# Kernel optimization log

Measured on AMD Instinct MI355X. Metric: run time of the kernel, lower is better.

The kernel has to match this reference:

```python
import jax, jax.numpy as jnp
import numpy as np

B, E, K = 512, 4096, 1024      # batch, emb_dim, key_dim
M, L = 1024, 32                # mem_size, prompt_length
TOP_K = 4
EPS = 1e-12


def _l2norm(x, axis=-1):
    n = jnp.linalg.norm(x, axis=axis, keepdims=True)
    return x / jnp.maximum(n, EPS)


def setup_inputs() -> dict:
    key = jax.random.key(0)
    k1, k2, k3, k4 = jax.random.split(key, 4)
    return {
        "x_query": jax.random.normal(k1, (B, E), dtype=jnp.float32),
        "W_proj": jax.random.normal(k2, (K, E), dtype=jnp.float32) * 0.02,
        "prompt_memory": jax.random.normal(k3, (M, L, E), dtype=jnp.float32) * 0.02,
        "prompt_keys": jax.random.normal(k4, (M, K), dtype=jnp.float32) * 0.02,
        "top_k": TOP_K,
    }


def reference(x_query, W_proj, prompt_memory, prompt_keys, top_k):
    # x_proj = Linear(emb_dim -> key_dim, no bias): x @ W.T
    x_proj = jnp.einsum("be,ke->bk", x_query, W_proj)          # [B, K]
    x_norm = _l2norm(x_proj)                                     # [B, K]
    key_norm = _l2norm(prompt_keys)                              # [M, K]
    sim = jnp.einsum("bk,mk->bm", x_norm, key_norm)             # [B, M]
    _, idx = jax.lax.top_k(sim, top_k)                           # [B, top_k]
    sel_prompts = prompt_memory[idx]                             # [B, top_k, L, E]
    sel_keys = _l2norm(prompt_keys[idx], axis=2)                 # [B, top_k, K]
    refined = jnp.einsum("bk,btk->bt", x_norm, sel_keys)        # [B, top_k]
    w = jax.nn.softmax(refined, axis=1)                          # [B, top_k]
    # softmax-weighted sum over selected prompts
    out = jnp.einsum("btle,bt->ble", sel_prompts, w)            # [B, L, E]
    return out
```

## Files before the change

### kernel.cpp

```cpp
#include <hip/hip_runtime.h>
#include <math.h>

#define BDIM 512
#define EDIM 4096
#define KDIM 1024
#define MDIM 1024
#define LDIM 32
#define TOPK 4
#define EPSF 1e-12f

typedef __attribute__((ext_vector_type(8))) short short8;
typedef __attribute__((ext_vector_type(4))) float f32x4;

struct us4 { ushort x, y, z, w; };

__device__ inline ushort f2bf_rn(float x) {
    union { float f; unsigned u; } v; v.f = x;
    unsigned r = (v.u + 0x7FFF + ((v.u >> 16) & 1)) >> 16;
    return (ushort)r;
}
__device__ inline float bf2f(ushort h) {
    union { unsigned u; float f; } v; v.u = ((unsigned)h) << 16;
    return v.f;
}

__global__ __launch_bounds__(256)
void split_all_kernel(const float* __restrict__ xq, const float* __restrict__ wp,
                      const float* __restrict__ pk,
                      ushort* __restrict__ xq_h, ushort* __restrict__ xq_l,
                      ushort* __restrict__ wp_h, ushort* __restrict__ wp_l,
                      ushort* __restrict__ pk_h, ushort* __restrict__ pk_l,
                      float* __restrict__ kn)
{
    const int blk = blockIdx.x;
    const int t = threadIdx.x;
    const float* src; ushort* hi; ushort* lo; int base;
    bool do_norm = false; int rowbase = 0;
    if (blk < 512)       { src = xq; hi = xq_h; lo = xq_l; base = blk * 1024; }
    else if (blk < 1536) { src = wp; hi = wp_h; lo = wp_l; base = (blk - 512) * 1024; }
    else                 { src = pk; hi = pk_h; lo = pk_l; base = (blk - 1536) * 1024;
                           do_norm = true; rowbase = (blk - 1536) * 4; }

    __shared__ float wsum[4];
    const int lane = t & 63, wwid = t >> 6;

    #pragma unroll
    for (int it = 0; it < 4; ++it) {
        const int i = base + it * 256 + t;
        float4 v = ((const float4*)src)[i];
        us4 h, l;
        h.x = f2bf_rn(v.x); l.x = f2bf_rn(v.x - bf2f(h.x));
        h.y = f2bf_rn(v.y); l.y = f2bf_rn(v.y - bf2f(h.y));
        h.z = f2bf_rn(v.z); l.z = f2bf_rn(v.z - bf2f(h.z));
        h.w = f2bf_rn(v.w); l.w = f2bf_rn(v.w - bf2f(h.w));
        ((us4*)hi)[i] = h;
        ((us4*)lo)[i] = l;

        if (do_norm) {
            float sq = v.x * v.x + v.y * v.y + v.z * v.z + v.w * v.w;
            #pragma unroll
            for (int off = 32; off > 0; off >>= 1) sq += __shfl_down(sq, off, 64);
            __syncthreads();
            if (lane == 0) wsum[wwid] = sq;
            __syncthreads();
            if (t == 0)
                kn[rowbase + it] = sqrtf(wsum[0] + wsum[1] + wsum[2] + wsum[3]);
        }
    }
}

__global__ __launch_bounds__(256)
void gemm1_kernel(const ushort* __restrict__ Ah, const ushort* __restrict__ Al,
                  const ushort* __restrict__ Bh, const ushort* __restrict__ Bl,
                  float* __restrict__ Cp)
{
    __shared__ ushort ldsA[2][2][64][40];
    __shared__ ushort ldsB[2][2][128][40];

    const int t  = threadIdx.x;
    const int bn = blockIdx.x, bm = blockIdx.y, kz = blockIdx.z;
    const int srow = t >> 2, sg = t & 3;
    const int Kc = EDIM / 4;

    const size_t aoff  = (size_t)(bm * 64 + srow) * EDIM + kz * Kc + sg * 8;
    const size_t boff0 = (size_t)(bn * 128 + srow) * EDIM + kz * Kc + sg * 8;
    const size_t boff1 = (size_t)(bn * 128 + 64 + srow) * EDIM + kz * Kc + sg * 8;

    const int lane = t & 63, wid = t >> 6;
    const int wr = wid >> 1, wc = wid & 1;
    const int fr = lane & 15, fg = lane >> 4;

    f32x4 acc[2][4];
    #pragma unroll
    for (int i = 0; i < 2; ++i)
        #pragma unroll
        for (int j = 0; j < 4; ++j)
            acc[i][j] = (f32x4){0.f, 0.f, 0.f, 0.f};

    short8 pAh = *(const short8*)(Ah + aoff);
    short8 pAl = *(const short8*)(Al + aoff);
    short8 pBh0 = *(const short8*)(Bh + boff0);
    short8 pBl0 = *(const short8*)(Bl + boff0);
    short8 pBh1 = *(const short8*)(Bh + boff1);
    short8 pBl1 = *(const short8*)(Bl + boff1);

    *(short8*)(&ldsA[0][0][srow][sg * 8]) = pAh;
    *(short8*)(&ldsA[0][1][srow][sg * 8]) = pAl;
    *(short8*)(&ldsB[0][0][srow][sg * 8]) = pBh0;
    *(short8*)(&ldsB[0][1][srow][sg * 8]) = pBl0;
    *(short8*)(&ldsB[0][0][64 + srow][sg * 8]) = pBh1;
    *(short8*)(&ldsB[0][1][64 + srow][sg * 8]) = pBl1;

    int p = 0;
    for (int k0 = 0; k0 < Kc; k0 += 32) {
        const bool more = (k0 + 32 < Kc);
        if (more) {
            pAh = *(const short8*)(Ah + aoff + k0 + 32);
            pAl = *(const short8*)(Al + aoff + k0 + 32);
            pBh0 = *(const short8*)(Bh + boff0 + k0 + 32);
            pBl0 = *(const short8*)(Bl + boff0 + k0 + 32);
            pBh1 = *(const short8*)(Bh + boff1 + k0 + 32);
            pBl1 = *(const short8*)(Bl + boff1 + k0 + 32);
        }
        __syncthreads();

        short8 ah[2], al[2], bh[4], bl[4];
        #pragma unroll
        for (int i = 0; i < 2; ++i) {
            ah[i] = *(const short8*)(&ldsA[p][0][wr * 32 + i * 16 + fr][fg * 8]);
            al[i] = *(const short8*)(&ldsA[p][1][wr * 32 + i * 16 + fr][fg * 8]);
        }
        #pragma unroll
        for (int j = 0; j < 4; ++j) {
            bh[j] = *(const short8*)(&ldsB[p][0][wc * 64 + j * 16 + fr][fg * 8]);
            bl[j] = *(const short8*)(&ldsB[p][1][wc * 64 + j * 16 + fr][fg * 8]);
        }
        #pragma unroll
        for (int i = 0; i < 2; ++i)
            #pragma unroll
            for (int j = 0; j < 4; ++j) {
                acc[i][j] = __builtin_amdgcn_mfma_f32_16x16x32_bf16(ah[i], bh[j], acc[i][j], 0, 0, 0);
                acc[i][j] = __builtin_amdgcn_mfma_f32_16x16x32_bf16(ah[i], bl[j], acc[i][j], 0, 0, 0);
                acc[i][j] = __builtin_amdgcn_mfma_f32_16x16x32_bf16(al[i], bh[j], acc[i][j], 0, 0, 0);
            }

        if (more) {
            *(short8*)(&ldsA[p ^ 1][0][srow][sg * 8]) = pAh;
            *(short8*)(&ldsA[p ^ 1][1][srow][sg * 8]) = pAl;
            *(short8*)(&ldsB[p ^ 1][0][srow][sg * 8]) = pBh0;
            *(short8*)(&ldsB[p ^ 1][1][srow][sg * 8]) = pBl0;
            *(short8*)(&ldsB[p ^ 1][0][64 + srow][sg * 8]) = pBh1;
            *(short8*)(&ldsB[p ^ 1][1][64 + srow][sg * 8]) = pBl1;
        }
        p ^= 1;
    }

    float* Cz = Cp + (size_t)kz * BDIM * KDIM;
    #pragma unroll
    for (int i = 0; i < 2; ++i)
        #pragma unroll
        for (int j = 0; j < 4; ++j)
            #pragma unroll
            for (int q = 0; q < 4; ++q) {
                int orow = bm * 64 + wr * 32 + i * 16 + (lane >> 4) * 4 + q;
                int ocol = bn * 128 + wc * 64 + j * 16 + (lane & 15);
                Cz[(size_t)orow * KDIM + ocol] = acc[i][j][q];
            }
}

__global__ __launch_bounds__(256)
void gemm2_kernel(const ushort* __restrict__ Ah, const ushort* __restrict__ Al,
                  const ushort* __restrict__ Bh, const ushort* __restrict__ Bl,
                  float* __restrict__ Cp)
{
    __shared__ ushort lds[2][4][64][40];

    const int t  = threadIdx.x;
    const int bn = blockIdx.x, bm = blockIdx.y, kz = blockIdx.z;
    const int srow = t >> 2, sg = t & 3;
    const int Kc = KDIM / 2;

    const size_t aoff = (size_t)(bm * 64 + srow) * KDIM + kz * Kc + sg * 8;
    const size_t boff = (size_t)(bn * 64 + srow) * KDIM + kz * Kc + sg * 8;

    const int lane = t & 63, wid = t >> 6;
    const int wr = wid >> 1, wc = wid & 1;
    const int fr = lane & 15, fg = lane >> 4;

    f32x4 acc[2][2];
    #pragma unroll
    for (int i = 0; i < 2; ++i)
        #pragma unroll
        for (int j = 0; j < 2; ++j)
            acc[i][j] = (f32x4){0.f, 0.f, 0.f, 0.f};

    short8 pA0 = *(const short8*)(Ah + aoff);
    short8 pA1 = *(const short8*)(Al + aoff);
    short8 pB0 = *(const short8*)(Bh + boff);
    short8 pB1 = *(const short8*)(Bl + boff);

    *(short8*)(&lds[0][0][srow][sg * 8]) = pA0;
    *(short8*)(&lds[0][1][srow][sg * 8]) = pA1;
    *(short8*)(&lds[0][2][srow][sg * 8]) = pB0;
    *(short8*)(&lds[0][3][srow][sg * 8]) = pB1;

    int p = 0;
    for (int k0 = 0; k0 < Kc; k0 += 32) {
        const bool more = (k0 + 32 < Kc);
        if (more) {
            pA0 = *(const short8*)(Ah + aoff + k0 + 32);
            pA1 = *(const short8*)(Al + aoff + k0 + 32);
            pB0 = *(const short8*)(Bh + boff + k0 + 32);
            pB1 = *(const short8*)(Bl + boff + k0 + 32);
        }
        __syncthreads();

        short8 ah[2], al[2], bh[2], bl[2];
        #pragma unroll
        for (int i = 0; i < 2; ++i) {
            ah[i] = *(const short8*)(&lds[p][0][wr * 32 + i * 16 + fr][fg * 8]);
            al[i] = *(const short8*)(&lds[p][1][wr * 32 + i * 16 + fr][fg * 8]);
            bh[i] = *(const short8*)(&lds[p][2][wc * 32 + i * 16 + fr][fg * 8]);
            bl[i] = *(const short8*)(&lds[p][3][wc * 32 + i * 16 + fr][fg * 8]);
        }
        #pragma unroll
        for (int i = 0; i < 2; ++i)
            #pragma unroll
            for (int j = 0; j < 2; ++j) {
                acc[i][j] = __builtin_amdgcn_mfma_f32_16x16x32_bf16(ah[i], bh[j], acc[i][j], 0, 0, 0);
                acc[i][j] = __builtin_amdgcn_mfma_f32_16x16x32_bf16(ah[i], bl[j], acc[i][j], 0, 0, 0);
                acc[i][j] = __builtin_amdgcn_mfma_f32_16x16x32_bf16(al[i], bh[j], acc[i][j], 0, 0, 0);
            }

        if (more) {
            *(short8*)(&lds[p ^ 1][0][srow][sg * 8]) = pA0;
            *(short8*)(&lds[p ^ 1][1][srow][sg * 8]) = pA1;
            *(short8*)(&lds[p ^ 1][2][srow][sg * 8]) = pB0;
            *(short8*)(&lds[p ^ 1][3][srow][sg * 8]) = pB1;
        }
        p ^= 1;
    }

    float* Cz = Cp + (size_t)kz * BDIM * MDIM;
    #pragma unroll
    for (int i = 0; i < 2; ++i)
        #pragma unroll
        for (int j = 0; j < 2; ++j)
            #pragma unroll
            for (int q = 0; q < 4; ++q) {
                int orow = bm * 64 + wr * 32 + i * 16 + (lane >> 4) * 4 + q;
                int ocol = bn * 64 + wc * 32 + j * 16 + (lane & 15);
                Cz[(size_t)orow * MDIM + ocol] = acc[i][j][q];
            }
}

__global__ __launch_bounds__(256)
void reduce_split_norm_kernel(const float* __restrict__ Cp,
                              ushort* __restrict__ xh, ushort* __restrict__ xl,
                              float* __restrict__ xn)
{
    const int b = blockIdx.x;
    const int i = b * 256 + threadIdx.x;
    const int n4 = BDIM * KDIM / 4;

    float4 s = ((const float4*)Cp)[i];
    #pragma unroll
    for (int z = 1; z < 4; ++z) {
        float4 v = ((const float4*)Cp)[(size_t)z * n4 + i];
        s.x += v.x; s.y += v.y; s.z += v.z; s.w += v.w;
    }

    us4 h, l;
    h.x = f2bf_rn(s.x); l.x = f2bf_rn(s.x - bf2f(h.x));
    h.y = f2bf_rn(s.y); l.y = f2bf_rn(s.y - bf2f(h.y));
    h.z = f2bf_rn(s.z); l.z = f2bf_rn(s.z - bf2f(h.z));
    h.w = f2bf_rn(s.w); l.w = f2bf_rn(s.w - bf2f(h.w));
    ((us4*)xh)[i] = h;
    ((us4*)xl)[i] = l;

    float sq = s.x * s.x + s.y * s.y + s.z * s.z + s.w * s.w;
    #pragma unroll
    for (int off = 32; off > 0; off >>= 1) sq += __shfl_down(sq, off, 64);
    __shared__ float wsum[4];
    const int lane = threadIdx.x & 63, wwid = threadIdx.x >> 6;
    if (lane == 0) wsum[wwid] = sq;
    __syncthreads();
    if (threadIdx.x == 0)
        xn[b] = sqrtf(wsum[0] + wsum[1] + wsum[2] + wsum[3]);
}

__device__ inline bool tk_better(float x, int ix, float y, int iy) {
    return (x > y) || (x == y && ix < iy);
}
__device__ inline void tk_insert(float (&v)[4], int (&id)[4], float x, int m) {
    if (tk_better(x, m, v[3], id[3])) {
        v[3] = x; id[3] = m;
        if (tk_better(v[3], id[3], v[2], id[2])) {
            float tv = v[2]; int ti = id[2]; v[2] = v[3]; id[2] = id[3]; v[3] = tv; id[3] = ti;
            if (tk_better(v[2], id[2], v[1], id[1])) {
                tv = v[1]; ti = id[1]; v[1] = v[2]; id[1] = id[2]; v[2] = tv; id[2] = ti;
                if (tk_better(v[1], id[1], v[0], id[0])) {
                    tv = v[0]; ti = id[0]; v[0] = v[1]; id[0] = id[1]; v[1] = tv; id[1] = ti;
                }
            }
        }
    }
}
__global__ __launch_bounds__(256)
void topk_scale_kernel(const float* __restrict__ Cp2, const float* __restrict__ xn,
                       const float* __restrict__ kn,
                       int* __restrict__ topi, float* __restrict__ topw)
{
    const int b = blockIdx.x, t = threadIdx.x;
    const int lane = t & 63, wid = t >> 6;
    const float sb = 1.f / fmaxf(xn[b], EPSF);
    const float* r0 = Cp2 + (size_t)b * MDIM;
    const float* r1 = Cp2 + (size_t)BDIM * MDIM + (size_t)b * MDIM;

    float v[4] = {-INFINITY, -INFINITY, -INFINITY, -INFINITY};
    int id[4] = {-1, -1, -1, -1};
    #pragma unroll
    for (int j = 0; j < MDIM / 256; ++j) {
        int m = wid * 256 + j * 64 + lane;
        float s = (r0[m] + r1[m]) * sb / fmaxf(kn[m], EPSF);
        tk_insert(v, id, s, m);
    }
    for (int off = 32; off >= 1; off >>= 1) {
        float pv[4]; int pi[4];
        #pragma unroll
        for (int q = 0; q < 4; ++q) {
            pv[q] = __shfl_xor(v[q], off, 64);
            pi[q] = __shfl_xor(id[q], off, 64);
        }
        #pragma unroll
        for (int q = 0; q < 4; ++q) tk_insert(v, id, pv[q], pi[q]);
    }

    __shared__ float sv[4][4];
    __shared__ int   si[4][4];
    if (lane == 0) {
        #pragma unroll
        for (int q = 0; q < 4; ++q) { sv[wid][q] = v[q]; si[wid][q] = id[q]; }
    }
    __syncthreads();
    if (t == 0) {
        float fv[4] = {-INFINITY, -INFINITY, -INFINITY, -INFINITY};
        int   fi[4] = {-1, -1, -1, -1};
        #pragma unroll
        for (int w = 0; w < 4; ++w)
            #pragma unroll
            for (int q = 0; q < 4; ++q)
                tk_insert(fv, fi, sv[w][q], si[w][q]);

        const float mx = fmaxf(fmaxf(fv[0], fv[1]), fmaxf(fv[2], fv[3]));
        const float e0 = expf(fv[0] - mx), e1 = expf(fv[1] - mx);
        const float e2 = expf(fv[2] - mx), e3 = expf(fv[3] - mx);
        const float inv = 1.f / (e0 + e1 + e2 + e3);
        topw[b * 4 + 0] = e0 * inv; topw[b * 4 + 1] = e1 * inv;
        topw[b * 4 + 2] = e2 * inv; topw[b * 4 + 3] = e3 * inv;
        #pragma unroll
        for (int q = 0; q < 4; ++q) topi[b * 4 + q] = fi[q];
    }
}

__global__ __launch_bounds__(256)
void gather_out_kernel(const float* __restrict__ pm, const int* __restrict__ topi,
                       const float* __restrict__ topw, float* __restrict__ out)
{
    const int bl = blockIdx.x;
    const int b = bl & (BDIM - 1);
    const int l = bl >> 9;

    const int j0 = topi[b * 4 + 0], j1 = topi[b * 4 + 1], j2 = topi[b * 4 + 2], j3 = topi[b * 4 + 3];
    const float w0 = topw[b * 4 + 0], w1 = topw[b * 4 + 1], w2 = topw[b * 4 + 2], w3 = topw[b * 4 + 3];

    const f32x4* p0 = (const f32x4*)(pm + ((size_t)j0 * LDIM + l) * EDIM);
    const f32x4* p1 = (const f32x4*)(pm + ((size_t)j1 * LDIM + l) * EDIM);
    const f32x4* p2 = (const f32x4*)(pm + ((size_t)j2 * LDIM + l) * EDIM);
    const f32x4* p3 = (const f32x4*)(pm + ((size_t)j3 * LDIM + l) * EDIM);
    f32x4* o = (f32x4*)(out + ((size_t)b * LDIM + l) * EDIM);

    #pragma unroll
    for (int it = 0; it < EDIM / 4 / 256; ++it) {
        const int c = it * 256 + threadIdx.x;
        f32x4 a = p0[c], bb = p1[c], cc = p2[c], dd = p3[c];
        f32x4 r = w0 * a + w1 * bb + w2 * cc + w3 * dd;
        __builtin_nontemporal_store(r, &o[c]);
    }
}

extern "C" void kernel_launch(void* const* d_in, const int* in_sizes, int n_in,
                              void* d_out, int out_size, void* d_ws, size_t ws_size,
                              hipStream_t stream)
{
    const float* x_query = (const float*)d_in[0];
    const float* W_proj  = (const float*)d_in[1];
    const float* pm      = (const float*)d_in[2];
    const float* pkeys   = (const float*)d_in[3];
    float* out = (float*)d_out;

    char* w = (char*)d_ws;
    ushort* xq_h = (ushort*)w; w += (size_t)BDIM * EDIM * 2;
    ushort* xq_l = (ushort*)w; w += (size_t)BDIM * EDIM * 2;
    ushort* wp_h = (ushort*)w; w += (size_t)KDIM * EDIM * 2;
    ushort* wp_l = (ushort*)w; w += (size_t)KDIM * EDIM * 2;
    ushort* pk_h = (ushort*)w; w += (size_t)MDIM * KDIM * 2;
    ushort* pk_l = (ushort*)w; w += (size_t)MDIM * KDIM * 2;
    ushort* xp_h = (ushort*)w; w += (size_t)BDIM * KDIM * 2;
    ushort* xp_l = (ushort*)w; w += (size_t)BDIM * KDIM * 2;
    float* Cp1  = (float*)w; w += (size_t)4 * BDIM * KDIM * 4;
    float* Cp2  = (float*)w; w += (size_t)2 * BDIM * MDIM * 4;
    float* xn   = (float*)w; w += BDIM * 4;
    float* kn   = (float*)w; w += MDIM * 4;
    float* topw = (float*)w; w += BDIM * TOPK * 4;
    int*   topi = (int*)w;   w += BDIM * TOPK * 4;

    split_all_kernel<<<1792, 256, 0, stream>>>(
        x_query, W_proj, pkeys, xq_h, xq_l, wp_h, wp_l, pk_h, pk_l, kn);

    gemm1_kernel<<<dim3(KDIM / 128, BDIM / 64, 4), 256, 0, stream>>>(
        xq_h, xq_l, wp_h, wp_l, Cp1);

    reduce_split_norm_kernel<<<BDIM, 256, 0, stream>>>(Cp1, xp_h, xp_l, xn);

    gemm2_kernel<<<dim3(MDIM / 64, BDIM / 64, 2), 256, 0, stream>>>(
        xp_h, xp_l, pk_h, pk_l, Cp2);

    topk_scale_kernel<<<BDIM, 256, 0, stream>>>(Cp2, xn, kn, topi, topw);

    gather_out_kernel<<<BDIM * LDIM, 256, 0, stream>>>(pm, topi, topw, out);
}
```

Baseline: 234.6 us.

## Fuse bf16 hi/lo splitting into GEMM tile loads and drop split pass

The separate pre-pass that converted x_query, W_proj and prompt_keys into bf16 hi/lo arrays is removed. The GEMM kernels now load fp32 tiles and do the split in registers before writing to LDS. The prompt-key norms move into the reduction kernel as extra blocks. This saves one launch and the round trip of writing and rereading the split arrays. In exchange the GEMMs read twice as many bytes per tile, and every block that touches a tile redoes the split arithmetic.

Measured after the change: 233.9 us (median of 2 runs). Within noise of the previous version (-0.3%).

```diff
diff --git a/kernel.cpp b/kernel.cpp
--- a/kernel.cpp
+++ b/kernel.cpp
@@ -23,55 +23,20 @@
     union { unsigned u; float f; } v; v.u = ((unsigned)h) << 16;
     return v.f;
 }
+__device__ inline void split8(const float4& v0, const float4& v1,
+                              short8& h, short8& l)
+{
+    float f[8] = {v0.x, v0.y, v0.z, v0.w, v1.x, v1.y, v1.z, v1.w};
+    #pragma unroll
+    for (int e = 0; e < 8; ++e) {
+        ushort hh = f2bf_rn(f[e]);
+        h[e] = (short)hh;
+        l[e] = (short)f2bf_rn(f[e] - bf2f(hh));
+    }
+}
 
 __global__ __launch_bounds__(256)
-void split_all_kernel(const float* __restrict__ xq, const float* __restrict__ wp,
-                      const float* __restrict__ pk,
-                      ushort* __restrict__ xq_h, ushort* __restrict__ xq_l,
-                      ushort* __restrict__ wp_h, ushort* __restrict__ wp_l,
-                      ushort* __restrict__ pk_h, ushort* __restrict__ pk_l,
-                      float* __restrict__ kn)
-{
-    const int blk = blockIdx.x;
-    const int t = threadIdx.x;
-    const float* src; ushort* hi; ushort* lo; int base;
-    bool do_norm = false; int rowbase = 0;
-    if (blk < 512)       { src = xq; hi = xq_h; lo = xq_l; base = blk * 1024; }
-    else if (blk < 1536) { src = wp; hi = wp_h; lo = wp_l; base = (blk - 512) * 1024; }
-    else                 { src = pk; hi = pk_h; lo = pk_l; base = (blk - 1536) * 1024;
-                           do_norm = true; rowbase = (blk - 1536) * 4; }
-
-    __shared__ float wsum[4];
-    const int lane = t & 63, wwid = t >> 6;
-
-    #pragma unroll
-    for (int it = 0; it < 4; ++it) {
-        const int i = base + it * 256 + t;
-        float4 v = ((const float4*)src)[i];
-        us4 h, l;
-        h.x = f2bf_rn(v.x); l.x = f2bf_rn(v.x - bf2f(h.x));
-        h.y = f2bf_rn(v.y); l.y = f2bf_rn(v.y - bf2f(h.y));
-        h.z = f2bf_rn(v.z); l.z = f2bf_rn(v.z - bf2f(h.z));
-        h.w = f2bf_rn(v.w); l.w = f2bf_rn(v.w - bf2f(h.w));
-        ((us4*)hi)[i] = h;
-        ((us4*)lo)[i] = l;
-
-        if (do_norm) {
-            float sq = v.x * v.x + v.y * v.y + v.z * v.z + v.w * v.w;
-            #pragma unroll
-            for (int off = 32; off > 0; off >>= 1) sq += __shfl_down(sq, off, 64);
-            __syncthreads();
-            if (lane == 0) wsum[wwid] = sq;
-            __syncthreads();
-            if (t == 0)
-                kn[rowbase + it] = sqrtf(wsum[0] + wsum[1] + wsum[2] + wsum[3]);
-        }
-    }
-}
-
-__global__ __launch_bounds__(256)
-void gemm1_kernel(const ushort* __restrict__ Ah, const ushort* __restrict__ Al,
-                  const ushort* __restrict__ Bh, const ushort* __restrict__ Bl,
+void gemm1_kernel(const float* __restrict__ A, const float* __restrict__ B,
                   float* __restrict__ Cp)
 {
     __shared__ ushort ldsA[2][2][64][40];
@@ -97,30 +62,33 @@
         for (int j = 0; j < 4; ++j)
             acc[i][j] = (f32x4){0.f, 0.f, 0.f, 0.f};
 
-    short8 pAh = *(const short8*)(Ah + aoff);
-    short8 pAl = *(const short8*)(Al + aoff);
-    short8 pBh0 = *(const short8*)(Bh + boff0);
-    short8 pBl0 = *(const short8*)(Bl + boff0);
-    short8 pBh1 = *(const short8*)(Bh + boff1);
-    short8 pBl1 = *(const short8*)(Bl + boff1);
-
-    *(short8*)(&ldsA[0][0][srow][sg * 8]) = pAh;
-    *(short8*)(&ldsA[0][1][srow][sg * 8]) = pAl;
-    *(short8*)(&ldsB[0][0][srow][sg * 8]) = pBh0;
-    *(short8*)(&ldsB[0][1][srow][sg * 8]) = pBl0;
-    *(short8*)(&ldsB[0][0][64 + srow][sg * 8]) = pBh1;
-    *(short8*)(&ldsB[0][1][64 + srow][sg * 8]) = pBl1;
+    float4 a0 = *(const float4*)(A + aoff),  a1 = *(const float4*)(A + aoff + 4);
+    float4 b00 = *(const float4*)(B + boff0), b01 = *(const float4*)(B + boff0 + 4);
+    float4 b10 = *(const float4*)(B + boff1), b11 = *(const float4*)(B + boff1 + 4);
+
+    {
+        short8 hs, ls;
+        split8(a0, a1, hs, ls);
+        *(short8*)(&ldsA[0][0][srow][sg * 8]) = hs;
+        *(short8*)(&ldsA[0][1][srow][sg * 8]) = ls;
+        split8(b00, b01, hs, ls);
+        *(short8*)(&ldsB[0][0][srow][sg * 8]) = hs;
+        *(short8*)(&ldsB[0][1][srow][sg * 8]) = ls;
+        split8(b10, b11, hs, ls);
+        *(short8*)(&ldsB[0][0][64 + srow][sg * 8]) = hs;
+        *(short8*)(&ldsB[0][1][64 + srow][sg * 8]) = ls;
+    }
 
     int p = 0;
     for (int k0 = 0; k0 < Kc; k0 += 32) {
         const bool more = (k0 + 32 < Kc);
         if (more) {
-            pAh = *(const short8*)(Ah + aoff + k0 + 32);
-            pAl = *(const short8*)(Al + aoff + k0 + 32);
-            pBh0 = *(const short8*)(Bh + boff0 + k0 + 32);
-            pBl0 = *(const short8*)(Bl + boff0 + k0 + 32);
-            pBh1 = *(const short8*)(Bh + boff1 + k0 + 32);
-            pBl1 = *(const short8*)(Bl + boff1 + k0 + 32);
+            a0  = *(const float4*)(A + aoff + k0 + 32);
+            a1  = *(const float4*)(A + aoff + k0 + 36);
+            b00 = *(const float4*)(B + boff0 + k0 + 32);
+            b01 = *(const float4*)(B + boff0 + k0 + 36);
+            b10 = *(const float4*)(B + boff1 + k0 + 32);
+            b11 = *(const float4*)(B + boff1 + k0 + 36);
         }
         __syncthreads();
 
@@ -145,12 +113,16 @@
             }
 
         if (more) {
-            *(short8*)(&ldsA[p ^ 1][0][srow][sg * 8]) = pAh;
-            *(short8*)(&ldsA[p ^ 1][1][srow][sg * 8]) = pAl;
-            *(short8*)(&ldsB[p ^ 1][0][srow][sg * 8]) = pBh0;
-            *(short8*)(&ldsB[p ^ 1][1][srow][sg * 8]) = pBl0;
-            *(short8*)(&ldsB[p ^ 1][0][64 + srow][sg * 8]) = pBh1;
-            *(short8*)(&ldsB[p ^ 1][1][64 + srow][sg * 8]) = pBl1;
+            short8 hs, ls;
+            split8(a0, a1, hs, ls);
+            *(short8*)(&ldsA[p ^ 1][0][srow][sg * 8]) = hs;
+            *(short8*)(&ldsA[p ^ 1][1][srow][sg * 8]) = ls;
+            split8(b00, b01, hs, ls);
+            *(short8*)(&ldsB[p ^ 1][0][srow][sg * 8]) = hs;
+            *(short8*)(&ldsB[p ^ 1][1][srow][sg * 8]) = ls;
+            split8(b10, b11, hs, ls);
+            *(short8*)(&ldsB[p ^ 1][0][64 + srow][sg * 8]) = hs;
+            *(short8*)(&ldsB[p ^ 1][1][64 + srow][sg * 8]) = ls;
         }
         p ^= 1;
     }
@@ -169,9 +141,54 @@
 }
 
 __global__ __launch_bounds__(256)
+void reduce_split_norm_kernel(const float* __restrict__ Cp,
+                              const float* __restrict__ PK,
+                              ushort* __restrict__ xh, ushort* __restrict__ xl,
+                              float* __restrict__ xn, float* __restrict__ kn)
+{
+    const int blk = blockIdx.x, t = threadIdx.x;
+    float sq;
+    if (blk < BDIM) {
+        const int b = blk;
+        const int i = b * 256 + t;
+        const int n4 = BDIM * KDIM / 4;
+
+        float4 s = ((const float4*)Cp)[i];
+        #pragma unroll
+        for (int z = 1; z < 4; ++z) {
+            float4 v = ((const float4*)Cp)[(size_t)z * n4 + i];
+            s.x += v.x; s.y += v.y; s.z += v.z; s.w += v.w;
+        }
+
+        us4 h, l;
+        h.x = f2bf_rn(s.x); l.x = f2bf_rn(s.x - bf2f(h.x));
+        h.y = f2bf_rn(s.y); l.y = f2bf_rn(s.y - bf2f(h.y));
+        h.z = f2bf_rn(s.z); l.z = f2bf_rn(s.z - bf2f(h.z));
+        h.w = f2bf_rn(s.w); l.w = f2bf_rn(s.w - bf2f(h.w));
+        ((us4*)xh)[i] = h;
+        ((us4*)xl)[i] = l;
+
+        sq = s.x * s.x + s.y * s.y + s.z * s.z + s.w * s.w;
+    } else {
+        const int m = blk - BDIM;
+        float4 v = *(const float4*)(PK + (size_t)m * KDIM + t * 4);
+        sq = v.x * v.x + v.y * v.y + v.z * v.z + v.w * v.w;
+    }
+    #pragma unroll
+    for (int off = 32; off > 0; off >>= 1) sq += __shfl_down(sq, off, 64);
+    __shared__ float wsum[4];
+    const int lane = t & 63, wwid = t >> 6;
+    if (lane == 0) wsum[wwid] = sq;
+    __syncthreads();
+    if (t == 0) {
+        float r = sqrtf(wsum[0] + wsum[1] + wsum[2] + wsum[3]);
+        if (blk < BDIM) xn[blk] = r; else kn[blk - BDIM] = r;
+    }
+}
+
+__global__ __launch_bounds__(256)
 void gemm2_kernel(const ushort* __restrict__ Ah, const ushort* __restrict__ Al,
-                  const ushort* __restrict__ Bh, const ushort* __restrict__ Bl,
-                  float* __restrict__ Cp)
+                  const float* __restrict__ PK, float* __restrict__ Cp)
 {
     __shared__ ushort lds[2][4][64][40];
 
@@ -196,13 +213,17 @@
 
     short8 pA0 = *(const short8*)(Ah + aoff);
     short8 pA1 = *(const short8*)(Al + aoff);
-    short8 pB0 = *(const short8*)(Bh + boff);
-    short8 pB1 = *(const short8*)(Bl + boff);
-
-    *(short8*)(&lds[0][0][srow][sg * 8]) = pA0;
-    *(short8*)(&lds[0][1][srow][sg * 8]) = pA1;
-    *(short8*)(&lds[0][2][srow][sg * 8]) = pB0;
-    *(short8*)(&lds[0][3][srow][sg * 8]) = pB1;
+    float4 pb0 = *(const float4*)(PK + boff);
+    float4 pb1 = *(const float4*)(PK + boff + 4);
+
+    {
+        short8 hs, ls;
+        split8(pb0, pb1, hs, ls);
+        *(short8*)(&lds[0][0][srow][sg * 8]) = pA0;
+        *(short8*)(&lds[0][1][srow][sg * 8]) = pA1;
+        *(short8*)(&lds[0][2][srow][sg * 8]) = hs;
+        *(short8*)(&lds[0][3][srow][sg * 8]) = ls;
+    }
 
     int p = 0;
     for (int k0 = 0; k0 < Kc; k0 += 32) {
@@ -210,8 +231,8 @@
         if (more) {
             pA0 = *(const short8*)(Ah + aoff + k0 + 32);
             pA1 = *(const short8*)(Al + aoff + k0 + 32);
-            pB0 = *(const short8*)(Bh + boff + k0 + 32);
-            pB1 = *(const short8*)(Bl + boff + k0 + 32);
+            pb0 = *(const float4*)(PK + boff + k0 + 32);
+            pb1 = *(const float4*)(PK + boff + k0 + 36);
         }
         __syncthreads();
 
@@ -233,10 +254,12 @@
             }
 
         if (more) {
+            short8 hs, ls;
+            split8(pb0, pb1, hs, ls);
             *(short8*)(&lds[p ^ 1][0][srow][sg * 8]) = pA0;
             *(short8*)(&lds[p ^ 1][1][srow][sg * 8]) = pA1;
-            *(short8*)(&lds[p ^ 1][2][srow][sg * 8]) = pB0;
-            *(short8*)(&lds[p ^ 1][3][srow][sg * 8]) = pB1;
+            *(short8*)(&lds[p ^ 1][2][srow][sg * 8]) = hs;
+            *(short8*)(&lds[p ^ 1][3][srow][sg * 8]) = ls;
         }
         p ^= 1;
     }
@@ -252,41 +275,6 @@
                 int ocol = bn * 64 + wc * 32 + j * 16 + (lane & 15);
                 Cz[(size_t)orow * MDIM + ocol] = acc[i][j][q];
             }
-}
-
-__global__ __launch_bounds__(256)
-void reduce_split_norm_kernel(const float* __restrict__ Cp,
-                              ushort* __restrict__ xh, ushort* __restrict__ xl,
-                              float* __restrict__ xn)
-{
-    const int b = blockIdx.x;
-    const int i = b * 256 + threadIdx.x;
-    const int n4 = BDIM * KDIM / 4;
-
-    float4 s = ((const float4*)Cp)[i];
-    #pragma unroll
-    for (int z = 1; z < 4; ++z) {
-        float4 v = ((const float4*)Cp)[(size_t)z * n4 + i];
-        s.x += v.x; s.y += v.y; s.z += v.z; s.w += v.w;
-    }
-
-    us4 h, l;
-    h.x = f2bf_rn(s.x); l.x = f2bf_rn(s.x - bf2f(h.x));
-    h.y = f2bf_rn(s.y); l.y = f2bf_rn(s.y - bf2f(h.y));
-    h.z = f2bf_rn(s.z); l.z = f2bf_rn(s.z - bf2f(h.z));
-    h.w = f2bf_rn(s.w); l.w = f2bf_rn(s.w - bf2f(h.w));
-    ((us4*)xh)[i] = h;
-    ((us4*)xl)[i] = l;
-
-    float sq = s.x * s.x + s.y * s.y + s.z * s.z + s.w * s.w;
-    #pragma unroll
-    for (int off = 32; off > 0; off >>= 1) sq += __shfl_down(sq, off, 64);
-    __shared__ float wsum[4];
-    const int lane = threadIdx.x & 63, wwid = threadIdx.x >> 6;
-    if (lane == 0) wsum[wwid] = sq;
-    __syncthreads();
-    if (threadIdx.x == 0)
-        xn[b] = sqrtf(wsum[0] + wsum[1] + wsum[2] + wsum[3]);
 }
 
 __device__ inline bool tk_better(float x, int ix, float y, int iy) {
@@ -400,12 +388,6 @@
     float* out = (float*)d_out;
 
     char* w = (char*)d_ws;
-    ushort* xq_h = (ushort*)w; w += (size_t)BDIM * EDIM * 2;
-    ushort* xq_l = (ushort*)w; w += (size_t)BDIM * EDIM * 2;
-    ushort* wp_h = (ushort*)w; w += (size_t)KDIM * EDIM * 2;
-    ushort* wp_l = (ushort*)w; w += (size_t)KDIM * EDIM * 2;
-    ushort* pk_h = (ushort*)w; w += (size_t)MDIM * KDIM * 2;
-    ushort* pk_l = (ushort*)w; w += (size_t)MDIM * KDIM * 2;
     ushort* xp_h = (ushort*)w; w += (size_t)BDIM * KDIM * 2;
     ushort* xp_l = (ushort*)w; w += (size_t)BDIM * KDIM * 2;
     float* Cp1  = (float*)w; w += (size_t)4 * BDIM * KDIM * 4;
@@ -415,16 +397,14 @@
     float* topw = (float*)w; w += BDIM * TOPK * 4;
     int*   topi = (int*)w;   w += BDIM * TOPK * 4;
 
-    split_all_kernel<<<1792, 256, 0, stream>>>(
-        x_query, W_proj, pkeys, xq_h, xq_l, wp_h, wp_l, pk_h, pk_l, kn);
-
     gemm1_kernel<<<dim3(KDIM / 128, BDIM / 64, 4), 256, 0, stream>>>(
-        xq_h, xq_l, wp_h, wp_l, Cp1);
-
-    reduce_split_norm_kernel<<<BDIM, 256, 0, stream>>>(Cp1, xp_h, xp_l, xn);
+        x_query, W_proj, Cp1);
+
+    reduce_split_norm_kernel<<<BDIM + MDIM, 256, 0, stream>>>(
+        Cp1, pkeys, xp_h, xp_l, xn, kn);
 
     gemm2_kernel<<<dim3(MDIM / 64, BDIM / 64, 2), 256, 0, stream>>>(
-        xp_h, xp_l, pk_h, pk_l, Cp2);
+        xp_h, xp_l, pkeys, Cp2);
 
     topk_scale_kernel<<<BDIM, 256, 0, stream>>>(Cp2, xn, kn, topi, topw);
 
```
